# Kernel optimization log

Hardware: AMD Instinct MI355X
Metric: run time of the kernel (lower is better)

The kernel has to match this reference:

```python
import jax, jax.numpy as jnp
import numpy as np

NUM_BINS = 16
TAU = 0.05
EPS_SUM = 1e-8
EPS_LOG = 1e-10


def _entropy(counts):
    # counts: (dim, bins) -> (dim,) entropy in bits
    probs = counts / jnp.clip(counts.sum(axis=-1, keepdims=True), EPS_SUM, None)
    return -(probs * jnp.log2(probs + EPS_LOG)).sum(axis=-1)


def setup_inputs() -> dict:
    key = jax.random.key(0)
    k1, k2 = jax.random.split(key)
    dim = 2097152
    observation = jax.random.normal(k1, (8, dim), dtype=jnp.float32)
    # positive histogram counts (buffer starts at ones in torch; randomize for a nontrivial test)
    belief_counts = jax.random.uniform(k2, (dim, NUM_BINS), dtype=jnp.float32)
    return {"observation": observation, "belief_counts": belief_counts}


def reference(observation, belief_counts):
    if observation.ndim == 2:
        observation = observation.mean(axis=0)  # (dim,)
    dim = observation.shape[0]

    prior_probs = belief_counts / jnp.clip(
        belief_counts.sum(axis=-1, keepdims=True), EPS_SUM, None)

    # sigmoid binning -> int bin indices in [0, NUM_BINS-1]
    normalized = jax.nn.sigmoid(observation)
    bins = jnp.clip((normalized * (NUM_BINS - 1)).astype(jnp.int32), 0, NUM_BINS - 1)

    one_hot = jax.nn.one_hot(bins, NUM_BINS, dtype=belief_counts.dtype)  # (dim, bins)
    posterior_counts = belief_counts + one_hot
    posterior_probs = posterior_counts / jnp.clip(
        posterior_counts.sum(axis=-1, keepdims=True), EPS_SUM, None)

    H_prior = _entropy(belief_counts)
    H_posterior = _entropy(posterior_counts)

    info_gain = jnp.clip(
        (posterior_probs * jnp.log2((posterior_probs + EPS_LOG) / (prior_probs + EPS_LOG))).sum(axis=-1),
        0.0, None)
    mean_info_gain = info_gain.mean()
    epistemic_value = jax.nn.sigmoid(mean_info_gain * 50.0 - 1.0)

    # EMA buffer update (no_grad in torch)
    new_belief_counts = jnp.clip(belief_counts * (1.0 - TAU) + one_hot * TAU, 0.01, None)

    return (info_gain, mean_info_gain, H_prior, H_posterior, epistemic_value,
            new_belief_counts)
```

## Files before the change

kernel.cpp:

```cpp
#include <hip/hip_runtime.h>
#include <math.h>

namespace {
constexpr int   NUM_BINS = 16;
constexpr float TAU      = 0.05f;
constexpr float EPS_SUM  = 1e-8f;
constexpr float EPS_LOG  = 1e-10f;
constexpr int   BLOCK    = 256;
constexpr int   GRID     = 2048;
}

__device__ inline float quad_sum(float x) {
    int a = __builtin_amdgcn_mov_dpp(__float_as_int(x), 0xB1, 0xF, 0xF, true);
    x += __int_as_float(a);
    a = __builtin_amdgcn_mov_dpp(__float_as_int(x), 0x4E, 0xF, 0xF, true);
    x += __int_as_float(a);
    return x;
}

__device__ inline float fast_log2(float x) { return __log2f(x); }
__device__ inline float fast_rcp(float x)  { return __builtin_amdgcn_rcpf(x); }

__global__ __launch_bounds__(BLOCK) void ev_main(
    const float* __restrict__ obs,
    const float* __restrict__ belief,
    float* __restrict__ out_info,
    float* __restrict__ out_Hprior,
    float* __restrict__ out_Hpost,
    float* __restrict__ out_newbelief,
    float* __restrict__ ws_partials,
    int dim)
{
    const int tid    = blockIdx.x * BLOCK + threadIdx.x;
    const int stride = BLOCK * GRID;
    const int W      = dim * 4;
    float local_sum = 0.0f;

    const float4* belief4 = reinterpret_cast<const float4*>(belief);
    float2* nb2 = reinterpret_cast<float2*>(out_newbelief);

#pragma unroll 4
    for (int f = tid; f < W; f += stride) {
        const int r = f >> 2;
        const int m = f & 3;

        float4 c4 = belief4[f];
        float cs = (c4.x + c4.y) + (c4.z + c4.w);
        float os = obs[(size_t)(2 * m) * dim + r]
                 + obs[(size_t)(2 * m + 1) * dim + r];

        cs = quad_sum(cs);
        os = quad_sum(os);
        float om = os * 0.125f;

        float sig = 1.0f / (1.0f + expf(-om));
        int bin = (int)(sig * 15.0f);
        bin = bin < 0 ? 0 : (bin > 15 ? 15 : bin);

        float inv_prior = fast_rcp(fmaxf(cs, EPS_SUM));
        float inv_post  = fast_rcp(fmaxf(cs + 1.0f, EPS_SUM));

        float Hpr = 0.0f, Hpo = 0.0f, ig = 0.0f;
        float cc[4] = {c4.x, c4.y, c4.z, c4.w};
        float nb[4];
        const int j0 = m * 4;
#pragma unroll
        for (int e = 0; e < 4; ++e) {
            float cj = cc[e];
            bool hit = (j0 + e == bin);
            float oh = hit ? 1.0f : 0.0f;
            float p  = cj * inv_prior;
            float pp = (cj + oh) * inv_post;
            float lp  = fast_log2(p  + EPS_LOG);
            float lpp = fast_log2(pp + EPS_LOG);
            Hpr -= p  * lp;
            Hpo -= pp * lpp;
            ig  += pp * (lpp - lp);
            nb[e] = fmaxf(fmaf(cj, 1.0f - TAU, hit ? TAU : 0.0f), 0.01f);
        }
        Hpr = quad_sum(Hpr);
        Hpo = quad_sum(Hpo);
        ig  = fmaxf(quad_sum(ig), 0.0f);
        local_sum += ig;

        if (m == 0) {
            out_info[r]   = ig;
            out_Hprior[r] = Hpr;
            out_Hpost[r]  = Hpo;
        }

        nb2[(size_t)f * 2]     = make_float2(nb[0], nb[1]);
        nb2[(size_t)f * 2 + 1] = make_float2(nb[2], nb[3]);
    }

    __shared__ float sdata[BLOCK];
    sdata[threadIdx.x] = local_sum;
    __syncthreads();
#pragma unroll
    for (int off = BLOCK / 2; off > 0; off >>= 1) {
        if (threadIdx.x < off) sdata[threadIdx.x] += sdata[threadIdx.x + off];
        __syncthreads();
    }
    if (threadIdx.x == 0) ws_partials[blockIdx.x] = sdata[0];
}

__global__ __launch_bounds__(BLOCK) void ev_finalize(
    const float* __restrict__ ws_partials,
    float* __restrict__ out_mean,
    float* __restrict__ out_epi,
    int n_partials, float inv_cnt)
{
    float s = 0.0f;
    for (int i = threadIdx.x; i < n_partials; i += BLOCK) s += ws_partials[i];
    __shared__ float sdata[BLOCK];
    sdata[threadIdx.x] = s;
    __syncthreads();
#pragma unroll
    for (int off = BLOCK / 2; off > 0; off >>= 1) {
        if (threadIdx.x < off) sdata[threadIdx.x] += sdata[threadIdx.x + off];
        __syncthreads();
    }
    if (threadIdx.x == 0) {
        float mean = sdata[0] * inv_cnt;
        *out_mean = mean;
        *out_epi  = 1.0f / (1.0f + expf(-(mean * 50.0f - 1.0f)));
    }
}

extern "C" void kernel_launch(void* const* d_in, const int* in_sizes, int n_in,
                              void* d_out, int out_size, void* d_ws, size_t ws_size,
                              hipStream_t stream)
{
    const float* obs    = (const float*)d_in[0];
    const float* belief = (const float*)d_in[1];
    const int dim = in_sizes[0] / 8;

    float* o             = (float*)d_out;
    float* out_info      = o;
    float* out_mean      = o + dim;
    float* out_Hprior    = o + dim + 1;
    float* out_Hpost     = o + 2 * (size_t)dim + 1;
    float* out_epi       = o + 3 * (size_t)dim + 1;
    float* out_newbelief = o + 3 * (size_t)dim + 2;

    float* partials = (float*)d_ws;

    ev_main<<<GRID, BLOCK, 0, stream>>>(obs, belief, out_info, out_Hprior,
                                        out_Hpost, out_newbelief, partials, dim);
    ev_finalize<<<1, BLOCK, 0, stream>>>(partials, out_mean, out_epi, GRID,
                                         1.0f / (4.0f * (float)dim));
}
```

Before: 319.6 us.

## Split bin computation into separate kernel and software-pipeline belief loads

Adds a pre-pass kernel that reads the eight observation rows with float4 loads and writes one bin index per element to workspace. The main kernel then reads the belief tile plus one bin value instead of strided observation loads, and it double-buffers loads across two strided iterations with a sched barrier. This aims to improve load coalescing and hide memory latency. The cost is an extra launch and an extra write and read of a dim-sized bin array. A fused fallback is kept for when the workspace is too small.

```diff
diff --git a/kernel.cpp b/kernel.cpp
--- a/kernel.cpp
+++ b/kernel.cpp
@@ -2,7 +2,6 @@
 #include <math.h>
 
 namespace {
-constexpr int   NUM_BINS = 16;
 constexpr float TAU      = 0.05f;
 constexpr float EPS_SUM  = 1e-8f;
 constexpr float EPS_LOG  = 1e-10f;
@@ -21,7 +20,169 @@
 __device__ inline float fast_log2(float x) { return __log2f(x); }
 __device__ inline float fast_rcp(float x)  { return __builtin_amdgcn_rcpf(x); }
 
+__device__ __forceinline__ float bin_from8(float o0, float o1, float o2, float o3,
+                                           float o4, float o5, float o6, float o7) {
+    float x0 = o0 + o1, x1 = o2 + o3, x2 = o4 + o5, x3 = o6 + o7;
+    float os = (x0 + x1) + (x2 + x3);
+    float om = os * 0.125f;
+    float sig = 1.0f / (1.0f + expf(-om));
+    int bin = (int)(sig * 15.0f);
+    bin = bin < 0 ? 0 : (bin > 15 ? 15 : bin);
+    return (float)bin;
+}
+
+__global__ __launch_bounds__(BLOCK) void ev_bins(
+    const float* __restrict__ obs,
+    float* __restrict__ bins,
+    int dim)
+{
+    const int gid = blockIdx.x * BLOCK + threadIdx.x;
+    const int gstride = BLOCK * gridDim.x;
+    const int total4 = dim >> 2;
+    const size_t d4 = (size_t)total4;
+    const float4* obs4 = reinterpret_cast<const float4*>(obs);
+    float4* bins4 = reinterpret_cast<float4*>(bins);
+
+    for (int c = gid; c < total4; c += gstride) {
+        float4 r0 = obs4[0 * d4 + c];
+        float4 r1 = obs4[1 * d4 + c];
+        float4 r2 = obs4[2 * d4 + c];
+        float4 r3 = obs4[3 * d4 + c];
+        float4 r4 = obs4[4 * d4 + c];
+        float4 r5 = obs4[5 * d4 + c];
+        float4 r6 = obs4[6 * d4 + c];
+        float4 r7 = obs4[7 * d4 + c];
+        float4 b;
+        b.x = bin_from8(r0.x, r1.x, r2.x, r3.x, r4.x, r5.x, r6.x, r7.x);
+        b.y = bin_from8(r0.y, r1.y, r2.y, r3.y, r4.y, r5.y, r6.y, r7.y);
+        b.z = bin_from8(r0.z, r1.z, r2.z, r3.z, r4.z, r5.z, r6.z, r7.z);
+        b.w = bin_from8(r0.w, r1.w, r2.w, r3.w, r4.w, r5.w, r6.w, r7.w);
+        bins4[c] = b;
+    }
+    for (int c = total4 * 4 + gid; c < dim; c += gstride) {
+        bins[c] = bin_from8(obs[0 * (size_t)dim + c], obs[1 * (size_t)dim + c],
+                            obs[2 * (size_t)dim + c], obs[3 * (size_t)dim + c],
+                            obs[4 * (size_t)dim + c], obs[5 * (size_t)dim + c],
+                            obs[6 * (size_t)dim + c], obs[7 * (size_t)dim + c]);
+    }
+}
+
+__device__ __forceinline__ void process_item(
+    int f, float4 c4, int bin,
+    float* __restrict__ out_info, float* __restrict__ out_Hprior,
+    float* __restrict__ out_Hpost, float2* __restrict__ nb2,
+    float& local_sum)
+{
+    const int r = f >> 2;
+    const int m = f & 3;
+
+    float cs = quad_sum((c4.x + c4.y) + (c4.z + c4.w));
+
+    float inv_prior = fast_rcp(fmaxf(cs, EPS_SUM));
+    float inv_post  = fast_rcp(fmaxf(cs + 1.0f, EPS_SUM));
+
+    float Hpr = 0.0f, Hpo = 0.0f, ig = 0.0f;
+    float cc[4] = {c4.x, c4.y, c4.z, c4.w};
+    float nb[4];
+    const int j0 = m * 4;
+#pragma unroll
+    for (int e = 0; e < 4; ++e) {
+        float cj = cc[e];
+        bool hit = (j0 + e == bin);
+        float oh = hit ? 1.0f : 0.0f;
+        float p  = cj * inv_prior;
+        float pp = (cj + oh) * inv_post;
+        float lp  = fast_log2(p  + EPS_LOG);
+        float lpp = fast_log2(pp + EPS_LOG);
+        Hpr -= p  * lp;
+        Hpo -= pp * lpp;
+        ig  += pp * (lpp - lp);
+        nb[e] = fmaxf(fmaf(cj, 1.0f - TAU, hit ? TAU : 0.0f), 0.01f);
+    }
+    Hpr = quad_sum(Hpr);
+    Hpo = quad_sum(Hpo);
+    ig  = fmaxf(quad_sum(ig), 0.0f);
+    local_sum += ig;
+
+    if (m == 0) {
+        out_info[r]   = ig;
+        out_Hprior[r] = Hpr;
+        out_Hpost[r]  = Hpo;
+    }
+    nb2[(size_t)f * 2]     = make_float2(nb[0], nb[1]);
+    nb2[(size_t)f * 2 + 1] = make_float2(nb[2], nb[3]);
+}
+
 __global__ __launch_bounds__(BLOCK) void ev_main(
+    const float* __restrict__ belief,
+    const float* __restrict__ binsf,
+    float* __restrict__ out_info,
+    float* __restrict__ out_Hprior,
+    float* __restrict__ out_Hpost,
+    float* __restrict__ out_newbelief,
+    float* __restrict__ ws_partials,
+    int dim)
+{
+    const int tid    = blockIdx.x * BLOCK + threadIdx.x;
+    const int stride = BLOCK * GRID;
+    const int W      = dim * 4;
+    const int step2  = 2 * stride;
+    const int Wbulk  = W - (W % step2);
+    float local_sum = 0.0f;
+
+    const float4* belief4 = reinterpret_cast<const float4*>(belief);
+    float2* nb2 = reinterpret_cast<float2*>(out_newbelief);
+
+    int f = tid;
+    float4 A0, A1;
+    float b0, b1;
+    if (f < Wbulk) {
+        A0 = belief4[f];
+        b0 = binsf[f >> 2];
+        A1 = belief4[f + stride];
+        b1 = binsf[(f + stride) >> 2];
+    }
+
+    for (; f < Wbulk; f += step2) {
+        const int fp = f + step2;
+        const bool more = (fp < Wbulk);
+        const int g0 = more ? fp : f;
+        const int g1 = more ? fp + stride : f;
+        float4 P0 = belief4[g0];
+        float  p0 = binsf[g0 >> 2];
+        float4 P1 = belief4[g1];
+        float  p1 = binsf[g1 >> 2];
+
+        __builtin_amdgcn_sched_barrier(0);
+
+        process_item(f,          A0, (int)b0,
+                     out_info, out_Hprior, out_Hpost, nb2, local_sum);
+        process_item(f + stride, A1, (int)b1,
+                     out_info, out_Hprior, out_Hpost, nb2, local_sum);
+
+        A0 = P0; b0 = p0;
+        A1 = P1; b1 = p1;
+    }
+
+    for (; f < W; f += stride) {
+        float4 c4 = belief4[f];
+        int bin = (int)binsf[f >> 2];
+        process_item(f, c4, bin,
+                     out_info, out_Hprior, out_Hpost, nb2, local_sum);
+    }
+
+    __shared__ float sdata[BLOCK];
+    sdata[threadIdx.x] = local_sum;
+    __syncthreads();
+#pragma unroll
+    for (int off = BLOCK / 2; off > 0; off >>= 1) {
+        if (threadIdx.x < off) sdata[threadIdx.x] += sdata[threadIdx.x + off];
+        __syncthreads();
+    }
+    if (threadIdx.x == 0) ws_partials[blockIdx.x] = sdata[0];
+}
+
+__global__ __launch_bounds__(BLOCK) void ev_fused(
     const float* __restrict__ obs,
     const float* __restrict__ belief,
     float* __restrict__ out_info,
@@ -39,58 +200,19 @@
     const float4* belief4 = reinterpret_cast<const float4*>(belief);
     float2* nb2 = reinterpret_cast<float2*>(out_newbelief);
 
-#pragma unroll 4
     for (int f = tid; f < W; f += stride) {
         const int r = f >> 2;
         const int m = f & 3;
-
         float4 c4 = belief4[f];
-        float cs = (c4.x + c4.y) + (c4.z + c4.w);
-        float os = obs[(size_t)(2 * m) * dim + r]
-                 + obs[(size_t)(2 * m + 1) * dim + r];
-
-        cs = quad_sum(cs);
-        os = quad_sum(os);
+        float oa = obs[(size_t)(2 * m) * dim + r];
+        float ob = obs[(size_t)(2 * m + 1) * dim + r];
+        float os = quad_sum(oa + ob);
         float om = os * 0.125f;
-
         float sig = 1.0f / (1.0f + expf(-om));
         int bin = (int)(sig * 15.0f);
         bin = bin < 0 ? 0 : (bin > 15 ? 15 : bin);
-
-        float inv_prior = fast_rcp(fmaxf(cs, EPS_SUM));
-        float inv_post  = fast_rcp(fmaxf(cs + 1.0f, EPS_SUM));
-
-        float Hpr = 0.0f, Hpo = 0.0f, ig = 0.0f;
-        float cc[4] = {c4.x, c4.y, c4.z, c4.w};
-        float nb[4];
-        const int j0 = m * 4;
-#pragma unroll
-        for (int e = 0; e < 4; ++e) {
-            float cj = cc[e];
-            bool hit = (j0 + e == bin);
-            float oh = hit ? 1.0f : 0.0f;
-            float p  = cj * inv_prior;
-            float pp = (cj + oh) * inv_post;
-            float lp  = fast_log2(p  + EPS_LOG);
-            float lpp = fast_log2(pp + EPS_LOG);
-            Hpr -= p  * lp;
-            Hpo -= pp * lpp;
-            ig  += pp * (lpp - lp);
-            nb[e] = fmaxf(fmaf(cj, 1.0f - TAU, hit ? TAU : 0.0f), 0.01f);
-        }
-        Hpr = quad_sum(Hpr);
-        Hpo = quad_sum(Hpo);
-        ig  = fmaxf(quad_sum(ig), 0.0f);
-        local_sum += ig;
-
-        if (m == 0) {
-            out_info[r]   = ig;
-            out_Hprior[r] = Hpr;
-            out_Hpost[r]  = Hpo;
-        }
-
-        nb2[(size_t)f * 2]     = make_float2(nb[0], nb[1]);
-        nb2[(size_t)f * 2 + 1] = make_float2(nb[2], nb[3]);
+        process_item(f, c4, bin,
+                     out_info, out_Hprior, out_Hpost, nb2, local_sum);
     }
 
     __shared__ float sdata[BLOCK];
@@ -144,9 +266,19 @@
     float* out_newbelief = o + 3 * (size_t)dim + 2;
 
     float* partials = (float*)d_ws;
-
-    ev_main<<<GRID, BLOCK, 0, stream>>>(obs, belief, out_info, out_Hprior,
-                                        out_Hpost, out_newbelief, partials, dim);
+    float* bins     = (float*)d_ws + GRID;
+    const size_t ws_needed = sizeof(float) * ((size_t)GRID + (size_t)dim);
+
+    if (ws_size >= ws_needed) {
+        ev_bins<<<GRID, BLOCK, 0, stream>>>(obs, bins, dim);
+        ev_main<<<GRID, BLOCK, 0, stream>>>(belief, bins, out_info, out_Hprior,
+                                            out_Hpost, out_newbelief, partials,
+                                            dim);
+    } else {
+        ev_fused<<<GRID, BLOCK, 0, stream>>>(obs, belief, out_info, out_Hprior,
+                                             out_Hpost, out_newbelief, partials,
+                                             dim);
+    }
     ev_finalize<<<1, BLOCK, 0, stream>>>(partials, out_mean, out_epi, GRID,
                                          1.0f / (4.0f * (float)dim));
 }
```

Result: faster. 313.2 us (-2.0%).
